# Kernel optimization log

Hardware: AMD Instinct MI355X
Metric: run time of the kernel (lower is better)

The kernel has to match this reference:

```python
import math
import jax, jax.numpy as jnp
import numpy as np

WINDOW_SHAPE = [30, 30, 8]
DEPTH = 8
NUM_DIMS = 3
N_POINTS = 2_000_000
BATCH = 4
SPARSE_SHAPE = np.array([32, 512, 512], dtype=np.int64)  # [D, H, W]


def _right_shift_bits(b, k):
    # shift bit-array right along last axis: prepend k zeros, drop last k
    if b.shape[-1] <= k:
        return jnp.zeros_like(b)
    pad = [(0, 0)] * (b.ndim - 1) + [(k, 0)]
    return jnp.pad(b[..., :-k], pad)


def _gray2binary(gray):
    # prefix-XOR along last axis via doubling (matches torch gray2binary)
    n = gray.shape[-1]
    shift = 2 ** (math.ceil(math.log2(n)) - 1)
    while shift > 0:
        gray = jnp.logical_xor(gray, _right_shift_bits(gray, shift))
        shift //= 2
    return gray


def hilbert_encode(locs, num_dims, num_bits):
    # locs: [N, num_dims] int, each in [0, 2**num_bits)
    n = locs.shape[0]
    # bit b of gray is the (num_bits-1-b)-th bit of the coordinate (MSB first)
    shifts_ = (num_bits - 1 - jnp.arange(num_bits, dtype=locs.dtype))
    gray = ((locs[:, :, None] >> shifts_[None, None, :]) & 1).astype(bool)  # [N, D, B]
    # Skilling's transform: small fixed loop (num_bits*num_dims = 24 iters)
    for bit in range(num_bits):
        for dim in range(num_dims):
            mask = gray[:, dim, bit]  # [N]
            g0 = jnp.logical_xor(gray[:, 0, bit + 1:], mask[:, None])
            gray = gray.at[:, 0, bit + 1:].set(g0)
            to_flip = jnp.logical_and(
                jnp.logical_not(mask)[:, None],
                jnp.logical_xor(gray[:, 0, bit + 1:], gray[:, dim, bit + 1:]),
            )
            gray = gray.at[:, dim, bit + 1:].set(
                jnp.logical_xor(gray[:, dim, bit + 1:], to_flip))
            gray = gray.at[:, 0, bit + 1:].set(
                jnp.logical_xor(gray[:, 0, bit + 1:], to_flip))
    # interleave: swapaxes(1,2) then flatten -> [N, num_bits*num_dims], MSB first
    bits = jnp.transpose(gray, (0, 2, 1)).reshape(n, num_bits * num_dims)
    hb = _gray2binary(bits)
    nb = num_bits * num_dims
    weights = jnp.asarray((1 << (nb - 1 - np.arange(nb))), dtype=jnp.int32)
    code = (hb.astype(jnp.int32) * weights).sum(-1)
    return code


def setup_inputs() -> dict:
    key = jax.random.key(0)
    kb, kz, ky, kx = jax.random.split(key, 4)
    D, H, W = [int(v) for v in SPARSE_SHAPE]
    b = jax.random.randint(kb, (N_POINTS,), 0, BATCH, dtype=jnp.int32)
    z = jax.random.randint(kz, (N_POINTS,), 0, D, dtype=jnp.int32)
    y = jax.random.randint(ky, (N_POINTS,), 0, H, dtype=jnp.int32)
    x = jax.random.randint(kx, (N_POINTS,), 0, W, dtype=jnp.int32)
    coords = jnp.stack([b, z, y, x], axis=-1)  # [N, 4]: bs, z, y, x
    return {"coords": coords, "sparse_shape": SPARSE_SHAPE, "shifts": 1}


def reference(coords, sparse_shape, shifts):
    # sparse_shape is static config: [D, H, W]; reversed -> W, H, D (as in torch)
    ss = [int(v) for v in np.asarray(sparse_shape)][::-1]
    W, H, D = ss
    wx, wy, wz = WINDOW_SHAPE
    if bool(shifts):
        sx, sy, sz = math.ceil(wx / 2), math.ceil(wy / 2), math.ceil(wz / 2)
    else:
        sx = sy = sz = 0
    b = coords[:, 0]
    x = (coords[:, 3] + sx) % W
    y = (coords[:, 2] + sy) % H
    z = (coords[:, 1] + sz) % D
    locs = jnp.stack([x, y, z], axis=-1)  # [N, 3]
    code = hilbert_encode(locs, NUM_DIMS, DEPTH)
    code = code | (b.astype(code.dtype) << (DEPTH * 3))
    coords2curve = jnp.argsort(code)
    return coords2curve
```

## Files before the change

### kernel.cpp

```cpp
#include <hip/hip_runtime.h>
#include <stdint.h>


#define THREADS 512
#define TILE 4096
#define TILE2 8192
#define WAVES (THREADS / 64)
#define IDX_BITS 22
#define IDX_MASK 0x3FFFFFu

__device__ __forceinline__ int tile_of(int bid, int nwg) {
  int q = nwg >> 3, r = nwg & 7;
  int x = bid & 7, k = bid >> 3;
  return x * q + (x < r ? x : r) + k;
}

__device__ __forceinline__ uint32_t hilbert_code(uint32_t x, uint32_t y, uint32_t z) {
  uint32_t X0 = x & 255u, X1 = y & 255u, X2 = z & 255u;
#pragma unroll
  for (int p = 7; p >= 0; --p) {
    uint32_t low = (1u << p) - 1u;
    uint32_t f0 = (uint32_t)-(int)((X0 >> p) & 1u);
    X0 ^= (low & f0);
    uint32_t f1 = (uint32_t)-(int)((X1 >> p) & 1u);
    uint32_t t1 = ((X0 ^ X1) & low) & ~f1;
    X0 ^= (low & f1) ^ t1;
    X1 ^= t1;
    uint32_t f2 = (uint32_t)-(int)((X2 >> p) & 1u);
    uint32_t t2 = ((X0 ^ X2) & low) & ~f2;
    X0 ^= (low & f2) ^ t2;
    X2 ^= t2;
  }
  uint32_t G = 0;
#pragma unroll
  for (int k = 0; k < 8; ++k) {
    int p = 7 - k;
    G |= ((X0 >> p) & 1u) << (23 - 3 * k);
    G |= ((X1 >> p) & 1u) << (22 - 3 * k);
    G |= ((X2 >> p) & 1u) << (21 - 3 * k);
  }
  G ^= G >> 16; G ^= G >> 8; G ^= G >> 4; G ^= G >> 2; G ^= G >> 1;
  return G & 0xFFFFFFu;
}

__global__ __launch_bounds__(THREADS) void genkeys_hist(
    const int4* __restrict__ coords, const void* __restrict__ ss,
    const int* __restrict__ shifts, uint32_t* __restrict__ keys0,
    int* __restrict__ hist, int N) {
  __shared__ int lh[512];
  int t = threadIdx.x, b = tile_of(blockIdx.x, gridDim.x);
  lh[t] = 0;

  const int* p32 = (const int*)ss;
  int D, H, W;
  if (p32[1] == 0) { const long long* p64 = (const long long*)ss;
    D = (int)p64[0]; H = (int)p64[1]; W = (int)p64[2]; }
  else { D = p32[0]; H = p32[1]; W = p32[2]; }
  int sflag = shifts[0];
  int sx = sflag ? 15 : 0, sy = sflag ? 15 : 0, sz = sflag ? 4 : 0;
  bool wp2 = (W & (W - 1)) == 0, hp2 = (H & (H - 1)) == 0, dp2 = (D & (D - 1)) == 0;
  __syncthreads();

#pragma unroll
  for (int r = 0; r < TILE / THREADS; ++r) {
    int idx = b * TILE + r * THREADS + t;
    if (idx < N) {
      int4 c = coords[idx];
      uint32_t bb = (uint32_t)c.x;
      int zz = c.y + sz, yy = c.z + sy, xx = c.w + sx;
      uint32_t z = (uint32_t)(dp2 ? (zz & (D - 1)) : (zz % D));
      uint32_t y = (uint32_t)(hp2 ? (yy & (H - 1)) : (yy % H));
      uint32_t x = (uint32_t)(wp2 ? (xx & (W - 1)) : (xx % W));
      uint32_t code = hilbert_code(x, y, z) | (bb << 24);
      keys0[idx] = code;
      atomicAdd(&lh[code & 511u], 1);
    }
  }
  __syncthreads();
  hist[(size_t)b * 512 + t] = lh[t];
}

template <int SHIFT, int NB, int TB>
__global__ __launch_bounds__(THREADS) void hist_kernel(
    const uint32_t* __restrict__ keys, int* __restrict__ hist, int N) {
  __shared__ int lh[NB];
  int t = threadIdx.x, b = tile_of(blockIdx.x, gridDim.x);
  if (t < NB) lh[t] = 0;
  __syncthreads();
#pragma unroll
  for (int r = 0; r < TB / THREADS / 4; ++r) {
    int base = b * TB + (r * THREADS + t) * 4;
    if (base + 3 < N) {
      uint4 k = *(const uint4*)(keys + base);
      atomicAdd(&lh[(k.x >> SHIFT) & (NB - 1)], 1);
      atomicAdd(&lh[(k.y >> SHIFT) & (NB - 1)], 1);
      atomicAdd(&lh[(k.z >> SHIFT) & (NB - 1)], 1);
      atomicAdd(&lh[(k.w >> SHIFT) & (NB - 1)], 1);
    } else {
      for (int u = 0; u < 4; ++u)
        if (base + u < N) atomicAdd(&lh[(keys[base + u] >> SHIFT) & (NB - 1)], 1);
    }
  }
  __syncthreads();
  if (t < NB) hist[(size_t)b * NB + t] = lh[t];
}

__global__ __launch_bounds__(512) void scan_blocks(
    int* __restrict__ hist, int* __restrict__ digitTotals, int nblocks, int nbins) {
  __shared__ int wsum[8];
  int d = blockIdx.x, t = threadIdx.x, wave = t >> 6, lane = t & 63;
  int carry = 0;
  for (int start = 0; start < nblocks; start += 512) {
    int i = start + t;
    int vv = (i < nblocks) ? hist[(size_t)i * nbins + d] : 0;
    int x = vv;
#pragma unroll
    for (int off = 1; off < 64; off <<= 1) {
      int n = __shfl_up(x, off);
      if (lane >= off) x += n;
    }
    if (lane == 63) wsum[wave] = x;
    __syncthreads();
    int pre = 0;
    for (int w = 0; w < wave; ++w) pre += wsum[w];
    if (i < nblocks) hist[(size_t)i * nbins + d] = carry + pre + x - vv;
    int tot = 0;
    for (int w = 0; w < 8; ++w) tot += wsum[w];
    __syncthreads();
    carry += tot;
  }
  if (t == 0) digitTotals[d] = carry;
}

template <int MODE>
__global__ __launch_bounds__(THREADS) void scatter_kernel(
    const uint32_t* __restrict__ in0, const uint32_t* __restrict__ in1,
    uint32_t* __restrict__ out0, uint32_t* __restrict__ out1,
    const int* __restrict__ hist, const int* __restrict__ digitTotals, int N) {
  constexpr int NB = (MODE == 2) ? 256 : 512;
  constexpr int RB = (MODE == 2) ? 8 : 9;
  constexpr int SHIFT = (MODE == 0) ? 0 : (MODE == 1) ? 9 : 22;
  constexpr int TB = (MODE == 2) ? TILE2 : TILE;
  constexpr int RNDS = TB / THREADS;
  constexpr int CH = TB / WAVES;
  __shared__ uint64_t sbuf[TB <= 4096 ? TB : TB / 2];
  __shared__ __align__(16) unsigned short cnt[WAVES][NB];
  int t = threadIdx.x, b = tile_of(blockIdx.x, gridDim.x);
  int wave = t >> 6, lane = t & 63;

  int histv = 0, dt = 0;
  if (t < NB) {
    histv = hist[(size_t)b * NB + t];
    dt = digitTotals[t];
  }
  for (int i = t; i < WAVES * NB; i += THREADS) ((unsigned short*)cnt)[i] = 0;
  __syncthreads();

  uint32_t kR[RNDS];
  uint32_t vR[(MODE == 1) ? RNDS : 1];
  int drR[RNDS];
  uint64_t ltm = (1ull << lane) - 1ull;
  int chunk0 = b * TB + wave * CH;

#pragma unroll
  for (int r = 0; r < RNDS; ++r) {
    int idx = chunk0 + r * 64 + lane;
    bool valid = idx < N;
    uint32_t a = valid ? in0[idx] : 0u;
    kR[r] = a;
    if (MODE == 1) vR[r] = valid ? in1[idx] : 0u;
    int digit = (int)((a >> SHIFT) & (NB - 1));
    uint64_t eq = __ballot(valid);
#pragma unroll
    for (int bit = 0; bit < RB; ++bit) {
      uint64_t m = __ballot((digit >> bit) & 1);
      eq &= ((digit >> bit) & 1) ? m : ~m;
    }
    int waveRank = __popcll(eq & ltm);
    int cntW = __popcll(eq);
    int prior = cnt[wave][digit];
    drR[r] = valid ? (digit | ((prior + waveRank) << RB)) : -1;
    if (valid && waveRank == 0) cnt[wave][digit] = (unsigned short)(prior + cntW);
  }
  __syncthreads();

  int2* wt = (int2*)sbuf;
  int tot = 0, adjv = 0;
  int2 v = make_int2(0, 0);
  if (t < NB) {
#pragma unroll
    for (int w = 0; w < WAVES; ++w) tot += cnt[w][t];
    v = make_int2(tot, dt);
#pragma unroll
    for (int off = 1; off < 64; off <<= 1) {
      int nx = __shfl_up(v.x, off), ny = __shfl_up(v.y, off);
      if (lane >= off) { v.x += nx; v.y += ny; }
    }
    if (lane == 63) wt[wave] = v;
  }
  __syncthreads();
  if (t < NB) {
    int2 pre = make_int2(0, 0);
    for (int w = 0; w < wave; ++w) { pre.x += wt[w].x; pre.y += wt[w].y; }
    int ds = pre.x + v.x - tot;
    adjv = histv + (pre.y + v.y - dt) - ds;
    int run = ds;
#pragma unroll
    for (int w = 0; w < WAVES; ++w) {
      int x = cnt[w][t];
      cnt[w][t] = (unsigned short)run;
      run += x;
    }
  }
  __syncthreads();

#pragma unroll
  for (int r = 0; r < RNDS; ++r) {
    int dr = drR[r];
    if (dr >= 0) {
      int digit = dr & (NB - 1);
      int rnk = dr >> RB;
      int slot = (int)cnt[wave][digit] + rnk;
      if (MODE == 0) {
        uint32_t idxv = (uint32_t)(chunk0 + r * 64 + lane);
        sbuf[slot] = ((uint64_t)idxv << 32) | kR[r];
      } else if (MODE == 1) {
        sbuf[slot] = ((uint64_t)vR[r] << 32) | kR[r];
      } else {
        ((uint32_t*)sbuf)[slot] = kR[r];
      }
    }
  }
  __syncthreads();

  int* adjArr = (int*)cnt;
  if (t < NB) adjArr[t] = adjv;
  __syncthreads();

  int validCount = min(TB, N - b * TB);
#pragma unroll
  for (int j = 0; j < RNDS; ++j) {
    int i = j * THREADS + t;
    if (i < validCount) {
      if (MODE == 0) {
        uint64_t kv = sbuf[i];
        uint32_t key = (uint32_t)kv;
        int pos = adjArr[key & 511u] + i;
        out0[pos] = key;
        out1[pos] = (uint32_t)(kv >> 32);
      } else if (MODE == 1) {
        uint64_t kv = sbuf[i];
        uint32_t key = (uint32_t)kv, idxv = (uint32_t)(kv >> 32);
        int pos = adjArr[(key >> 9) & 511u] + i;
        out0[pos] = ((key >> 18) << IDX_BITS) | idxv;
      } else {
        uint32_t p = ((uint32_t*)sbuf)[i];
        int pos = adjArr[(p >> IDX_BITS) & 255u] + i;
        out0[pos] = p & IDX_MASK;
      }
    }
  }
}

extern "C" void kernel_launch(void* const* d_in, const int* in_sizes, int n_in,
                              void* d_out, int out_size, void* d_ws, size_t ws_size,
                              hipStream_t stream) {
  const int4* coords = (const int4*)d_in[0];
  const void* ss = d_in[1];
  const int* shifts = (const int*)d_in[2];
  int N = in_sizes[0] / 4;
  int nblocks = (N + TILE - 1) / TILE;
  int nblocks2 = (N + TILE2 - 1) / TILE2;

  char* ws = (char*)d_ws;
  size_t off = 0;
  auto alloc = [&](size_t bytes) -> void* {
    void* p = ws + off;
    off += (bytes + 255) & ~(size_t)255;
    return p;
  };
  uint32_t* keys0 = (uint32_t*)alloc((size_t)N * 4);
  uint32_t* keys1 = (uint32_t*)alloc((size_t)N * 4);
  uint32_t* vals1 = (uint32_t*)alloc((size_t)N * 4);
  uint32_t* packd = (uint32_t*)alloc((size_t)N * 4);
  int*      hist  = (int*)alloc((size_t)512 * nblocks * 4);
  int*      digitTotals = (int*)alloc(512 * 4);

  genkeys_hist<<<nblocks, THREADS, 0, stream>>>(coords, ss, shifts, keys0, hist, N);
  scan_blocks<<<512, 512, 0, stream>>>(hist, digitTotals, nblocks, 512);
  scatter_kernel<0><<<nblocks, THREADS, 0, stream>>>(
      keys0, nullptr, keys1, vals1, hist, digitTotals, N);

  hist_kernel<9, 512, TILE><<<nblocks, THREADS, 0, stream>>>(keys1, hist, N);
  scan_blocks<<<512, 512, 0, stream>>>(hist, digitTotals, nblocks, 512);
  scatter_kernel<1><<<nblocks, THREADS, 0, stream>>>(
      keys1, vals1, packd, nullptr, hist, digitTotals, N);

  hist_kernel<22, 256, TILE2><<<nblocks2, THREADS, 0, stream>>>(packd, hist, N);
  scan_blocks<<<256, 512, 0, stream>>>(hist, digitTotals, nblocks2, 256);
  scatter_kernel<2><<<nblocks2, THREADS, 0, stream>>>(
      packd, nullptr, (uint32_t*)d_out, nullptr, hist, digitTotals, N);
}
```

Measured before the change: 83.27 us.

## Halve radix scatter tile size and split keygen histogram into two rows per block

Scatter tiles for the first two radix passes shrink from 4096 to 2048 keys, giving about twice as many workgroups. The key-generation kernel keeps 4096-key blocks but writes two 2048-row histograms so its output matches the smaller scatter tiles. The scatter loop is also split so all key and value loads are issued before the ballot ranking, which lets the loads overlap. The aim is higher occupancy and better latency hiding, at the cost of more histogram rows to scan and more per-block overhead.

```diff
diff --git a/kernel.cpp b/kernel.cpp
--- a/kernel.cpp
+++ b/kernel.cpp
@@ -3,7 +3,8 @@
 
 
 #define THREADS 512
-#define TILE 4096
+#define GTILE 4096
+#define TILE 2048
 #define TILE2 8192
 #define WAVES (THREADS / 64)
 #define IDX_BITS 22
@@ -47,9 +48,9 @@
     const int4* __restrict__ coords, const void* __restrict__ ss,
     const int* __restrict__ shifts, uint32_t* __restrict__ keys0,
     int* __restrict__ hist, int N) {
-  __shared__ int lh[512];
+  __shared__ int lh[2][512];
   int t = threadIdx.x, b = tile_of(blockIdx.x, gridDim.x);
-  lh[t] = 0;
+  lh[0][t] = 0; lh[1][t] = 0;
 
   const int* p32 = (const int*)ss;
   int D, H, W;
@@ -62,8 +63,8 @@
   __syncthreads();
 
 #pragma unroll
-  for (int r = 0; r < TILE / THREADS; ++r) {
-    int idx = b * TILE + r * THREADS + t;
+  for (int r = 0; r < GTILE / THREADS; ++r) {
+    int idx = b * GTILE + r * THREADS + t;
     if (idx < N) {
       int4 c = coords[idx];
       uint32_t bb = (uint32_t)c.x;
@@ -73,11 +74,12 @@
       uint32_t x = (uint32_t)(wp2 ? (xx & (W - 1)) : (xx % W));
       uint32_t code = hilbert_code(x, y, z) | (bb << 24);
       keys0[idx] = code;
-      atomicAdd(&lh[code & 511u], 1);
-    }
-  }
-  __syncthreads();
-  hist[(size_t)b * 512 + t] = lh[t];
+      atomicAdd(&lh[r >= (GTILE / THREADS / 2)][code & 511u], 1);
+    }
+  }
+  __syncthreads();
+  hist[(size_t)(2 * b) * 512 + t] = lh[0][t];
+  hist[(size_t)(2 * b + 1) * 512 + t] = lh[1][t];
 }
 
 template <int SHIFT, int NB, int TB>
@@ -166,10 +168,15 @@
   for (int r = 0; r < RNDS; ++r) {
     int idx = chunk0 + r * 64 + lane;
     bool valid = idx < N;
-    uint32_t a = valid ? in0[idx] : 0u;
-    kR[r] = a;
+    kR[r] = valid ? in0[idx] : 0u;
     if (MODE == 1) vR[r] = valid ? in1[idx] : 0u;
-    int digit = (int)((a >> SHIFT) & (NB - 1));
+  }
+
+#pragma unroll
+  for (int r = 0; r < RNDS; ++r) {
+    int idx = chunk0 + r * 64 + lane;
+    bool valid = idx < N;
+    int digit = (int)((kR[r] >> SHIFT) & (NB - 1));
     uint64_t eq = __ballot(valid);
 #pragma unroll
     for (int bit = 0; bit < RB; ++bit) {
@@ -269,7 +276,9 @@
   const void* ss = d_in[1];
   const int* shifts = (const int*)d_in[2];
   int N = in_sizes[0] / 4;
-  int nblocks = (N + TILE - 1) / TILE;
+  int nblocksG = (N + GTILE - 1) / GTILE;
+  int nrows0   = 2 * nblocksG;
+  int nblocks1 = (N + TILE - 1) / TILE;
   int nblocks2 = (N + TILE2 - 1) / TILE2;
 
   char* ws = (char*)d_ws;
@@ -283,17 +292,17 @@
   uint32_t* keys1 = (uint32_t*)alloc((size_t)N * 4);
   uint32_t* vals1 = (uint32_t*)alloc((size_t)N * 4);
   uint32_t* packd = (uint32_t*)alloc((size_t)N * 4);
-  int*      hist  = (int*)alloc((size_t)512 * nblocks * 4);
+  int*      hist  = (int*)alloc((size_t)512 * nrows0 * 4);
   int*      digitTotals = (int*)alloc(512 * 4);
 
-  genkeys_hist<<<nblocks, THREADS, 0, stream>>>(coords, ss, shifts, keys0, hist, N);
-  scan_blocks<<<512, 512, 0, stream>>>(hist, digitTotals, nblocks, 512);
-  scatter_kernel<0><<<nblocks, THREADS, 0, stream>>>(
+  genkeys_hist<<<nblocksG, THREADS, 0, stream>>>(coords, ss, shifts, keys0, hist, N);
+  scan_blocks<<<512, 512, 0, stream>>>(hist, digitTotals, nrows0, 512);
+  scatter_kernel<0><<<nblocks1, THREADS, 0, stream>>>(
       keys0, nullptr, keys1, vals1, hist, digitTotals, N);
 
-  hist_kernel<9, 512, TILE><<<nblocks, THREADS, 0, stream>>>(keys1, hist, N);
-  scan_blocks<<<512, 512, 0, stream>>>(hist, digitTotals, nblocks, 512);
-  scatter_kernel<1><<<nblocks, THREADS, 0, stream>>>(
+  hist_kernel<9, 512, TILE><<<nblocks1, THREADS, 0, stream>>>(keys1, hist, N);
+  scan_blocks<<<512, 512, 0, stream>>>(hist, digitTotals, nblocks1, 512);
+  scatter_kernel<1><<<nblocks1, THREADS, 0, stream>>>(
       keys1, vals1, packd, nullptr, hist, digitTotals, N);
 
   hist_kernel<22, 256, TILE2><<<nblocks2, THREADS, 0, stream>>>(packd, hist, N);
```

Result: slower. 88.45 us (+6.2%).
